# Kernel tuning notes

Hardware: AMD Instinct MI355X
Metric: run time of the kernel (lower is better)

Reference implementation:

```python
import jax, jax.numpy as jnp
import numpy as np


def setup_inputs() -> dict:
    key = jax.random.key(0)
    kq, kv = jax.random.split(key)
    B, Lq, Lv, H = 8, 2048, 2048, 256
    query = jax.random.normal(kq, (B, Lq, H), dtype=jnp.float32)
    value = jax.random.normal(kv, (B, Lv, H), dtype=jnp.float32)
    return {"query": query, "value": value}


def reference(query, value):
    # score[b, q, v] = sum_h query[b, q, h] * value[b, v, h]
    score = jnp.einsum("bqh,bvh->bqv", query, value)
    # softmax over the value axis (last dim), numerically stable
    attn = jax.nn.softmax(score, axis=-1)
    # context[b, q, h] = sum_v attn[b, q, v] * value[b, v, h]
    context = jnp.einsum("bqv,bvh->bqh", attn, value)
    return (context, attn)
```

## Files before the change

kernel.cpp:

```cpp
#include <hip/hip_runtime.h>
#include <hip/hip_bf16.h>

#define LQ 2048
#define LV 2048
#define NH 256
#define NB 8

typedef __attribute__((ext_vector_type(4))) float f32x4;
typedef __attribute__((ext_vector_type(8))) short bf16x8;

__device__ __forceinline__ ushort f32_bf16(float x) {
  union { float f; unsigned u; } c; c.f = x;
  unsigned r = (c.u + 0x7FFFu + ((c.u >> 16) & 1u)) >> 16;
  return (ushort)r;
}
__device__ __forceinline__ float bf16_f32(ushort h) {
  union { unsigned u; float f; } c; c.u = ((unsigned)h) << 16;
  return c.f;
}
__device__ __forceinline__ void gl_lds16(const ushort* g, ushort* l) {
  __builtin_amdgcn_global_load_lds(
      (const __attribute__((address_space(1))) unsigned int*)(g),
      (__attribute__((address_space(3))) unsigned int*)(l), 16, 0, 0);
}


__global__ __launch_bounds__(256) void k_prepQ(
    const float* __restrict__ Q, ushort* __restrict__ Qh, ushort* __restrict__ Ql) {
  int i = blockIdx.x * 256 + threadIdx.x;
  float4 x = reinterpret_cast<const float4*>(Q)[i];
  ushort4 h, l;
  h.x = f32_bf16(x.x); l.x = f32_bf16(x.x - bf16_f32(h.x));
  h.y = f32_bf16(x.y); l.y = f32_bf16(x.y - bf16_f32(h.y));
  h.z = f32_bf16(x.z); l.z = f32_bf16(x.z - bf16_f32(h.z));
  h.w = f32_bf16(x.w); l.w = f32_bf16(x.w - bf16_f32(h.w));
  reinterpret_cast<ushort4*>(Qh)[i] = h;
  reinterpret_cast<ushort4*>(Ql)[i] = l;
}

__global__ __launch_bounds__(256) void k_prepV(
    const float* __restrict__ V, ushort* __restrict__ Vh, ushort* __restrict__ Vl,
    ushort* __restrict__ VhT) {
  int id = blockIdx.x;
  int b = id & 7, vt = (id >> 3) & 31, ht = id >> 8;
  __shared__ ushort sT[64][72];
  int t = threadIdx.x;
  const size_t base = ((size_t)(b * LV) + vt * 64) * NH + ht * 64;
  int r0 = t >> 4, c4 = (t & 15) << 2;
  #pragma unroll
  for (int it = 0; it < 4; ++it) {
    int r = r0 + it * 16;
    size_t off = base + (size_t)r * NH + c4;
    float4 x = *reinterpret_cast<const float4*>(V + off);
    ushort4 h, l;
    h.x = f32_bf16(x.x); l.x = f32_bf16(x.x - bf16_f32(h.x));
    h.y = f32_bf16(x.y); l.y = f32_bf16(x.y - bf16_f32(h.y));
    h.z = f32_bf16(x.z); l.z = f32_bf16(x.z - bf16_f32(h.z));
    h.w = f32_bf16(x.w); l.w = f32_bf16(x.w - bf16_f32(h.w));
    *reinterpret_cast<ushort4*>(Vh + off) = h;
    *reinterpret_cast<ushort4*>(Vl + off) = l;
    *reinterpret_cast<ushort4*>(&sT[r][c4]) = h;
  }
  __syncthreads();
  int hh = t & 63, vc = t >> 6;
  ushort tmp[16];
  #pragma unroll
  for (int j = 0; j < 16; ++j) tmp[j] = sT[vc * 16 + j][hh];
  ushort* dst = VhT + ((size_t)(b * NH) + ht * 64 + hh) * LV + vt * 64 + vc * 16;
  *reinterpret_cast<ushort4*>(dst)      = *reinterpret_cast<ushort4*>(&tmp[0]);
  *reinterpret_cast<ushort4*>(dst + 4)  = *reinterpret_cast<ushort4*>(&tmp[4]);
  *reinterpret_cast<ushort4*>(dst + 8)  = *reinterpret_cast<ushort4*>(&tmp[8]);
  *reinterpret_cast<ushort4*>(dst + 12) = *reinterpret_cast<ushort4*>(&tmp[12]);
}

__global__ __launch_bounds__(512) void k_scores6(
    const ushort* __restrict__ Qh, const ushort* __restrict__ Ql,
    const ushort* __restrict__ Vh, const ushort* __restrict__ Vl,
    float* __restrict__ S, float2* __restrict__ PS) {
  extern __shared__ ushort dynlds[];
  int id = blockIdx.x;
  int b = id & 7, qt = (id >> 3) & 7, vt = id >> 6;
  int t = threadIdx.x, lane = t & 63, w = t >> 6;

  const size_t bq = (size_t)(b * LQ) + qt * 256;
  const size_t bv = (size_t)(b * LV) + vt * 256;

#define LBASE(buf, arr) ((char*)dynlds + ((buf) * 4 + (arr)) * (256 * 64))

#define STAGE(buf, kt)                                                      \
  {                                                                         \
    int krow = t >> 2, c = t & 3;                                           \
    _Pragma("unroll")                                                       \
    for (int hh = 0; hh < 2; ++hh) {                                        \
      int row = hh * 128 + krow;                                            \
      int csrc = c ^ ((row >> 1) & 3);                                      \
      size_t gq = (bq + row) * NH + (kt) * 32 + csrc * 8;                   \
      size_t gv = (bv + row) * NH + (kt) * 32 + csrc * 8;                   \
      gl_lds16(Qh + gq, (ushort*)(LBASE(buf, 0) + row * 64 + c * 16));      \
      gl_lds16(Ql + gq, (ushort*)(LBASE(buf, 1) + row * 64 + c * 16));      \
      gl_lds16(Vh + gv, (ushort*)(LBASE(buf, 2) + row * 64 + c * 16));      \
      gl_lds16(Vl + gv, (ushort*)(LBASE(buf, 3) + row * 64 + c * 16));      \
    }                                                                       \
  }

  int wq = w >> 1, wv = w & 1;
  int ar = wq * 64 + (lane & 15);
  int br = wv * 128 + (lane & 15);
  int kb = lane >> 4;

  f32x4 acc[4][8] = {};

  STAGE(0, 0);
  STAGE(1, 1);

  #pragma unroll
  for (int kt = 0; kt < 8; ++kt) {
    const int cur = kt & 1;
    if (kt < 7) { asm volatile("s_waitcnt vmcnt(8)" ::: "memory"); }
    else        { asm volatile("s_waitcnt vmcnt(0)" ::: "memory"); }
    __builtin_amdgcn_sched_barrier(0);
    __builtin_amdgcn_s_barrier();
    __builtin_amdgcn_sched_barrier(0);

    bf16x8 ah[4], al[4];
    #pragma unroll
    for (int m = 0; m < 4; ++m) {
      int r = ar + m * 16;
      int off = r * 64 + ((kb ^ ((r >> 1) & 3)) << 4);
      ah[m] = *reinterpret_cast<const bf16x8*>(LBASE(cur, 0) + off);
      al[m] = *reinterpret_cast<const bf16x8*>(LBASE(cur, 1) + off);
    }
    __builtin_amdgcn_s_setprio(1);
    #pragma unroll
    for (int n = 0; n < 8; ++n) {
      int r = br + n * 16;
      int off = r * 64 + ((kb ^ ((r >> 1) & 3)) << 4);
      bf16x8 bh = *reinterpret_cast<const bf16x8*>(LBASE(cur, 2) + off);
      bf16x8 bl = *reinterpret_cast<const bf16x8*>(LBASE(cur, 3) + off);
      #pragma unroll
      for (int m = 0; m < 4; ++m) {
        acc[m][n] = __builtin_amdgcn_mfma_f32_16x16x32_bf16(ah[m], bh, acc[m][n], 0, 0, 0);
        acc[m][n] = __builtin_amdgcn_mfma_f32_16x16x32_bf16(ah[m], bl, acc[m][n], 0, 0, 0);
        acc[m][n] = __builtin_amdgcn_mfma_f32_16x16x32_bf16(al[m], bh, acc[m][n], 0, 0, 0);
      }
    }
    __builtin_amdgcn_s_setprio(0);
    __builtin_amdgcn_sched_barrier(0);
    __builtin_amdgcn_s_barrier();
    __builtin_amdgcn_sched_barrier(0);
    if (kt < 6) STAGE(cur, kt + 2);
  }

  #pragma unroll
  for (int m = 0; m < 4; ++m) {
    #pragma unroll
    for (int j = 0; j < 4; ++j) {
      float mx = acc[m][0][j];
      #pragma unroll
      for (int n = 1; n < 8; ++n) mx = fmaxf(mx, acc[m][n][j]);
      #pragma unroll
      for (int off = 1; off < 16; off <<= 1) mx = fmaxf(mx, __shfl_xor(mx, off));
      float s = 0.f;
      #pragma unroll
      for (int n = 0; n < 8; ++n) s += __expf(acc[m][n][j] - mx);
      #pragma unroll
      for (int off = 1; off < 16; off <<= 1) s += __shfl_xor(s, off);
      if ((lane & 15) == 0) {
        int g = lane >> 4;
        int row = wq * 64 + m * 16 + g * 4 + j;
        float2 v; v.x = mx; v.y = s;
        PS[((size_t)(b * LQ) + qt * 256 + row) * 16 + vt * 2 + wv] = v;
      }
    }
  }

  float* Sp = S + (size_t)b * LQ * LV + (size_t)(qt * 256 + wq * 64) * LV
            + vt * 256 + wv * 128;
  int rb = (lane >> 4) << 2, c0 = lane & 15;
  #pragma unroll
  for (int m = 0; m < 4; ++m)
    #pragma unroll
    for (int j = 0; j < 4; ++j)
      #pragma unroll
      for (int n = 0; n < 8; ++n)
        Sp[(size_t)(m * 16 + rb + j) * LV + n * 16 + c0] = acc[m][n][j];
#undef STAGE
#undef LBASE
}

__global__ __launch_bounds__(512) void k_ctx8(
    const ushort* __restrict__ VhT, const float2* __restrict__ PS,
    float* __restrict__ A, float* __restrict__ C) {
  int id = blockIdx.x;
  int b = id & 7, qs = id >> 3;
  __shared__ float lm[32], li[32];
  __shared__ __align__(16) ushort sP[4][32 * 64];

  int t = threadIdx.x, lane = t & 63, w = t >> 6;
  float* Ab = A + (size_t)b * LQ * LV + (size_t)qs * 32 * LV;
  const ushort* Vb = VhT + (size_t)b * NH * LV;

  const int prow = t >> 4, pc = (t & 15) << 2;
  float* aaddr = Ab + (size_t)prow * LV + pc;
  const int poff = (prow * 128 + pc * 2) ^ ((prow & 7) << 4);

  {
    int row = t >> 4, seg = t & 15;
    float2 p = PS[((size_t)(b * LQ) + qs * 32 + row) * 16 + seg];
    float M = p.x, s = p.y;
    #pragma unroll
    for (int off = 1; off < 16; off <<= 1) {
      float mo = __shfl_xor(M, off), so = __shfl_xor(s, off);
      float mn = fmaxf(M, mo);
      s = s * __expf(M - mn) + so * __expf(mo - mn);
      M = mn;
    }
    if (seg == 0) { lm[row] = M; li[row] = 1.f / s; }
  }
  __syncthreads();

  const float pm = lm[prow], pinv = li[prow];

#define PRODUCE(xv, v0, buf)                                                \
  {                                                                         \
    float4 p;                                                               \
    p.x = __expf((xv).x - pm) * pinv; p.y = __expf((xv).y - pm) * pinv;     \
    p.z = __expf((xv).z - pm) * pinv; p.w = __expf((xv).w - pm) * pinv;     \
    *reinterpret_cast<float4*>(aaddr + (v0)) = p;                           \
    ushort4 pk;                                                             \
    pk.x = f32_bf16(p.x); pk.y = f32_bf16(p.y);                             \
    pk.z = f32_bf16(p.z); pk.w = f32_bf16(p.w);                             \
    *reinterpret_cast<ushort4*>((char*)&sP[buf][0] + poff) = pk;            \
  }

  float4 x0 = *reinterpret_cast<const float4*>(aaddr);
  float4 x1 = *reinterpret_cast<const float4*>(aaddr + 64);
  PRODUCE(x0, 0, 0);
  PRODUCE(x1, 64, 1);
  x0 = *reinterpret_cast<const float4*>(aaddr + 128);
  x1 = *reinterpret_cast<const float4*>(aaddr + 192);
  __syncthreads();

  f32x4 acc[2][2] = {};
  const int NP = LV / 128;

  for (int p = 0; p < NP; ++p) {
    const int cur = (p & 1) << 1;
    const int nxt = cur ^ 2;
    const int v0 = p * 128;
    if (p + 1 < NP) {
      PRODUCE(x0, v0 + 128, nxt);
      PRODUCE(x1, v0 + 192, nxt + 1);
    }
    if (p + 2 < NP) {
      x0 = *reinterpret_cast<const float4*>(aaddr + v0 + 256);
      x1 = *reinterpret_cast<const float4*>(aaddr + v0 + 320);
    }

    #pragma unroll
    for (int c = 0; c < 2; ++c) {
      #pragma unroll
      for (int ks = 0; ks < 2; ++ks) {
        int vbyte = ks * 64 + ((lane >> 4) << 4);
        bf16x8 pa[2];
        #pragma unroll
        for (int i2 = 0; i2 < 2; ++i2) {
          int arow = i2 * 16 + (lane & 15);
          pa[i2] = *reinterpret_cast<const bf16x8*>(
              (char*)&sP[cur + c][0] + ((arow * 128 + vbyte) ^ ((arow & 7) << 4)));
        }
        #pragma unroll
        for (int n = 0; n < 2; ++n) {
          int hrow = w * 32 + n * 16 + (lane & 15);
          bf16x8 vb = *reinterpret_cast<const bf16x8*>(
              Vb + (size_t)hrow * LV + v0 + c * 64 + ks * 32 + ((lane >> 4) << 3));
          #pragma unroll
          for (int i2 = 0; i2 < 2; ++i2)
            acc[i2][n] = __builtin_amdgcn_mfma_f32_16x16x32_bf16(pa[i2], vb, acc[i2][n], 0, 0, 0);
        }
      }
    }
    __syncthreads();
  }
#undef PRODUCE

  float* Cb = C + ((size_t)b * LQ + qs * 32) * NH + w * 32;
  int rb = (lane >> 4) << 2, c0 = lane & 15;
  #pragma unroll
  for (int i2 = 0; i2 < 2; ++i2)
    #pragma unroll
    for (int j = 0; j < 4; ++j)
      #pragma unroll
      for (int n = 0; n < 2; ++n)
        Cb[(size_t)(i2 * 16 + rb + j) * NH + n * 16 + c0] = acc[i2][n][j];
}


__global__ __launch_bounds__(256) void k_scores_fb(
    const float* __restrict__ Q, const float* __restrict__ V,
    float* __restrict__ S) {
  int id = blockIdx.x;
  int b = id & 7;
  int inner = id >> 3;
  int qt = inner & 31;
  int vt = inner >> 5;
  __shared__ ushort sQh[64 * 64], sQl[64 * 64], sVh[64 * 64], sVl[64 * 64];
  const float* Qb = Q + (size_t)(b * LQ + qt * 64) * NH;
  const float* Vb = V + (size_t)(b * LV + vt * 64) * NH;
  const int t = threadIdx.x;
  const int lane = t & 63;
  const int w = t >> 6;
  f32x4 acc[4] = {};
  const int row0 = t >> 4;
  const int col4 = (t & 15) << 2;
  for (int kc = 0; kc < 4; ++kc) {
    #pragma unroll
    for (int it = 0; it < 4; ++it) {
      int row = row0 + (it << 4);
      const float4 qx = *reinterpret_cast<const float4*>(Qb + (size_t)row * NH + kc * 64 + col4);
      const float4 vx = *reinterpret_cast<const float4*>(Vb + (size_t)row * NH + kc * 64 + col4);
      int off = ((row * 128 + col4 * 2) ^ ((row & 7) << 4)) >> 1;
      ushort4 h, l;
      h.x = f32_bf16(qx.x); l.x = f32_bf16(qx.x - bf16_f32(h.x));
      h.y = f32_bf16(qx.y); l.y = f32_bf16(qx.y - bf16_f32(h.y));
      h.z = f32_bf16(qx.z); l.z = f32_bf16(qx.z - bf16_f32(h.z));
      h.w = f32_bf16(qx.w); l.w = f32_bf16(qx.w - bf16_f32(h.w));
      *reinterpret_cast<ushort4*>(&sQh[off]) = h;
      *reinterpret_cast<ushort4*>(&sQl[off]) = l;
      h.x = f32_bf16(vx.x); l.x = f32_bf16(vx.x - bf16_f32(h.x));
      h.y = f32_bf16(vx.y); l.y = f32_bf16(vx.y - bf16_f32(h.y));
      h.z = f32_bf16(vx.z); l.z = f32_bf16(vx.z - bf16_f32(h.z));
      h.w = f32_bf16(vx.w); l.w = f32_bf16(vx.w - bf16_f32(h.w));
      *reinterpret_cast<ushort4*>(&sVh[off]) = h;
      *reinterpret_cast<ushort4*>(&sVl[off]) = l;
    }
    __syncthreads();
    int arow = (w << 4) + (lane & 15);
    int abase = arow * 128;
    int aswz = (arow & 7) << 4;
    #pragma unroll
    for (int ks = 0; ks < 2; ++ks) {
      int koffB = (ks << 6) + ((lane >> 4) << 4);
      int aoff = ((abase + koffB) ^ aswz) >> 1;
      bf16x8 ah = *reinterpret_cast<const bf16x8*>(&sQh[aoff]);
      bf16x8 al = *reinterpret_cast<const bf16x8*>(&sQl[aoff]);
      #pragma unroll
      for (int n = 0; n < 4; ++n) {
        int brow = (n << 4) + (lane & 15);
        int boff = (((brow * 128) + koffB) ^ ((brow & 7) << 4)) >> 1;
        bf16x8 bh = *reinterpret_cast<const bf16x8*>(&sVh[boff]);
        bf16x8 bl = *reinterpret_cast<const bf16x8*>(&sVl[boff]);
        acc[n] = __builtin_amdgcn_mfma_f32_16x16x32_bf16(ah, bh, acc[n], 0, 0, 0);
        acc[n] = __builtin_amdgcn_mfma_f32_16x16x32_bf16(ah, bl, acc[n], 0, 0, 0);
        acc[n] = __builtin_amdgcn_mfma_f32_16x16x32_bf16(al, bh, acc[n], 0, 0, 0);
      }
    }
    __syncthreads();
  }
  float* Sp = S + (size_t)b * LQ * LV + (size_t)(qt * 64) * LV + vt * 64;
  int rbase = (w << 4) + ((lane >> 4) << 2);
  int c0 = lane & 15;
  #pragma unroll
  for (int n = 0; n < 4; ++n)
    #pragma unroll
    for (int j = 0; j < 4; ++j)
      Sp[(size_t)(rbase + j) * LV + (n << 4) + c0] = acc[n][j];
}

__global__ __launch_bounds__(256) void k_stats_fb(const float* __restrict__ S,
                                                  float* __restrict__ ml) {
  const size_t r = blockIdx.x;
  const float* row = S + r * LV;
  int t = threadIdx.x;
  float4 a = *reinterpret_cast<const float4*>(row + (t << 2));
  float4 c = *reinterpret_cast<const float4*>(row + 1024 + (t << 2));
  float m = fmaxf(fmaxf(fmaxf(a.x, a.y), fmaxf(a.z, a.w)),
                  fmaxf(fmaxf(c.x, c.y), fmaxf(c.z, c.w)));
  #pragma unroll
  for (int off = 32; off; off >>= 1) m = fmaxf(m, __shfl_xor(m, off));
  __shared__ float redm[4];
  __shared__ float reds[4];
  if ((t & 63) == 0) redm[t >> 6] = m;
  __syncthreads();
  m = fmaxf(fmaxf(redm[0], redm[1]), fmaxf(redm[2], redm[3]));
  float s = __expf(a.x - m) + __expf(a.y - m) + __expf(a.z - m) + __expf(a.w - m)
          + __expf(c.x - m) + __expf(c.y - m) + __expf(c.z - m) + __expf(c.w - m);
  #pragma unroll
  for (int off = 32; off; off >>= 1) s += __shfl_xor(s, off);
  if ((t & 63) == 0) reds[t >> 6] = s;
  __syncthreads();
  if (t == 0) {
    float tot = reds[0] + reds[1] + reds[2] + reds[3];
    ml[2 * r] = m;
    ml[2 * r + 1] = 1.0f / tot;
  }
}

__global__ __launch_bounds__(256) void k_ctx_fb(
    const float* __restrict__ V, const float* __restrict__ ml,
    float* __restrict__ A, float* __restrict__ C) {
  int id = blockIdx.x;
  int b = id & 7;
  int qt = id >> 3;
  __shared__ ushort sP[32 * 40];
  __shared__ ushort sVT[256 * 40];
  __shared__ float lmv[32], liv[32];
  int t = threadIdx.x;
  int lane = t & 63;
  int w = t >> 6;
  int wr = w >> 1, wh = w & 1;
  if (t < 32) {
    size_t r = (size_t)b * LQ + qt * 32 + t;
    lmv[t] = ml[2 * r];
    liv[t] = ml[2 * r + 1];
  }
  __syncthreads();
  f32x4 acc[8] = {};
  float* Ab = A + (size_t)b * LQ * LV + (size_t)(qt * 32) * LV;
  const float* Vb = V + (size_t)b * LV * NH;
  const int prow = t >> 3;
  const int pv4 = (t & 7) << 2;
  for (int v0 = 0; v0 < LV; v0 += 32) {
    {
      float* addr = Ab + (size_t)prow * LV + v0 + pv4;
      float4 s4 = *reinterpret_cast<const float4*>(addr);
      float m = lmv[prow], inv = liv[prow];
      float4 p4;
      p4.x = __expf(s4.x - m) * inv;
      p4.y = __expf(s4.y - m) * inv;
      p4.z = __expf(s4.z - m) * inv;
      p4.w = __expf(s4.w - m) * inv;
      *reinterpret_cast<float4*>(addr) = p4;
      ushort4 pb;
      pb.x = f32_bf16(p4.x); pb.y = f32_bf16(p4.y);
      pb.z = f32_bf16(p4.z); pb.w = f32_bf16(p4.w);
      *reinterpret_cast<ushort4*>(&sP[prow * 40 + pv4]) = pb;
    }
    #pragma unroll 4
    for (int vl = 0; vl < 32; ++vl) {
      float x = Vb[(size_t)(v0 + vl) * NH + t];
      sVT[t * 40 + vl] = f32_bf16(x);
    }
    __syncthreads();
    bf16x8 pa = *reinterpret_cast<const bf16x8*>(
        &sP[((wr << 4) + (lane & 15)) * 40 + ((lane >> 4) << 3)]);
    #pragma unroll
    for (int n = 0; n < 8; ++n) {
      int hrow = (wh << 7) + (n << 4) + (lane & 15);
      bf16x8 vb = *reinterpret_cast<const bf16x8*>(
          &sVT[hrow * 40 + ((lane >> 4) << 3)]);
      acc[n] = __builtin_amdgcn_mfma_f32_16x16x32_bf16(pa, vb, acc[n], 0, 0, 0);
    }
    __syncthreads();
  }
  float* Cb = C + ((size_t)b * LQ + qt * 32) * NH;
  int rbase = (wr << 4) + ((lane >> 4) << 2);
  int c0 = lane & 15;
  #pragma unroll
  for (int n = 0; n < 8; ++n)
    #pragma unroll
    for (int j = 0; j < 4; ++j)
      Cb[(size_t)(rbase + j) * NH + (wh << 7) + (n << 4) + c0] = acc[n][j];
}


extern "C" void kernel_launch(void* const* d_in, const int* in_sizes, int n_in,
                              void* d_out, int out_size, void* d_ws, size_t ws_size,
                              hipStream_t stream) {
  const float* Q = (const float*)d_in[0];
  const float* V = (const float*)d_in[1];
  float* out = (float*)d_out;
  float* C = out;
  float* A = out + (size_t)NB * LQ * NH;

  const size_t NE = (size_t)NB * LQ * NH;
  const size_t PSN = (size_t)NB * LQ * 16;
  const size_t need = NE * 2 * 5 + PSN * 8;
  const int DYN_LDS = 2 * 4 * 256 * 32 * 2;

  bool big_lds_ok =
      hipFuncSetAttribute((const void*)k_scores6,
                          hipFuncAttributeMaxDynamicSharedMemorySize,
                          DYN_LDS) == hipSuccess;

  if (ws_size >= need && big_lds_ok) {
    ushort* Qh  = (ushort*)d_ws;
    ushort* Ql  = Qh + NE;
    ushort* Vh  = Ql + NE;
    ushort* Vl  = Vh + NE;
    ushort* VhT = Vl + NE;
    float2* PS  = (float2*)(VhT + NE);
    k_prepQ<<<dim3(NE / 4 / 256), dim3(256), 0, stream>>>(Q, Qh, Ql);
    k_prepV<<<dim3(NB * 32 * 4), dim3(256), 0, stream>>>(V, Vh, Vl, VhT);
    k_scores6<<<dim3(NB * 8 * 8), dim3(512), DYN_LDS, stream>>>(Qh, Ql, Vh, Vl, A, PS);
    k_ctx8<<<dim3(NB * 64), dim3(512), 0, stream>>>(VhT, PS, A, C);
  } else {
    float* ml = (float*)d_ws;
    k_scores_fb<<<dim3(NB * 32 * 32), dim3(256), 0, stream>>>(Q, V, A);
    k_stats_fb<<<dim3(NB * LQ), dim3(256), 0, stream>>>(A, ml);
    k_ctx_fb<<<dim3(NB * 64), dim3(256), 0, stream>>>(V, ml, A, C);
  }
}
```

Baseline: 161.1 us.

## Store unnormalized fp16 exp scores in-place to halve intermediate score traffic

The scores kernel now computes exp(score - local segment max) and writes it as fp16 into the upper half of each attention row, instead of writing raw fp32 scores. The context kernel reads these fp16 values and rescales them by a per-segment factor built from the partial max/sum stats. It then writes final fp32 probabilities in place. This cuts the bytes written and re-read for the large intermediate score matrix and drops the exp from the context kernel. In exchange it adds fp16 rounding and underflow on the probabilities, and it depends on in-place reads staying ahead of writes within each row.

```diff
diff --git a/kernel.cpp b/kernel.cpp
--- a/kernel.cpp
+++ b/kernel.cpp
@@ -17,6 +17,12 @@
 __device__ __forceinline__ float bf16_f32(ushort h) {
   union { unsigned u; float f; } c; c.u = ((unsigned)h) << 16;
   return c.f;
+}
+__device__ __forceinline__ ushort f32_f16(float x) {
+  union { _Float16 h; ushort u; } c; c.h = (_Float16)x; return c.u;
+}
+__device__ __forceinline__ float f16_f32(ushort u) {
+  union { ushort u; _Float16 h; } c; c.u = u; return (float)c.h;
 }
 __device__ __forceinline__ void gl_lds16(const ushort* g, ushort* l) {
   __builtin_amdgcn_global_load_lds(
@@ -73,7 +79,7 @@
   *reinterpret_cast<ushort4*>(dst + 12) = *reinterpret_cast<ushort4*>(&tmp[12]);
 }
 
-__global__ __launch_bounds__(512) void k_scores6(
+__global__ __launch_bounds__(512) void k_scores7(
     const ushort* __restrict__ Qh, const ushort* __restrict__ Ql,
     const ushort* __restrict__ Vh, const ushort* __restrict__ Vl,
     float* __restrict__ S, float2* __restrict__ PS) {
@@ -151,6 +157,7 @@
     if (kt < 6) STAGE(cur, kt + 2);
   }
 
+  const int g = lane >> 4, c0 = lane & 15;
   #pragma unroll
   for (int m = 0; m < 4; ++m) {
     #pragma unroll
@@ -160,40 +167,33 @@
       for (int n = 1; n < 8; ++n) mx = fmaxf(mx, acc[m][n][j]);
       #pragma unroll
       for (int off = 1; off < 16; off <<= 1) mx = fmaxf(mx, __shfl_xor(mx, off));
+      float e[8];
       float s = 0.f;
       #pragma unroll
-      for (int n = 0; n < 8; ++n) s += __expf(acc[m][n][j] - mx);
+      for (int n = 0; n < 8; ++n) { e[n] = __expf(acc[m][n][j] - mx); s += e[n]; }
       #pragma unroll
       for (int off = 1; off < 16; off <<= 1) s += __shfl_xor(s, off);
-      if ((lane & 15) == 0) {
-        int g = lane >> 4;
-        int row = wq * 64 + m * 16 + g * 4 + j;
+      int row = qt * 256 + wq * 64 + m * 16 + g * 4 + j;
+      if (c0 == 0) {
         float2 v; v.x = mx; v.y = s;
-        PS[((size_t)(b * LQ) + qt * 256 + row) * 16 + vt * 2 + wv] = v;
+        PS[((size_t)(b * LQ) + row) * 16 + vt * 2 + wv] = v;
       }
-    }
-  }
-
-  float* Sp = S + (size_t)b * LQ * LV + (size_t)(qt * 256 + wq * 64) * LV
-            + vt * 256 + wv * 128;
-  int rb = (lane >> 4) << 2, c0 = lane & 15;
-  #pragma unroll
-  for (int m = 0; m < 4; ++m)
-    #pragma unroll
-    for (int j = 0; j < 4; ++j)
-      #pragma unroll
-      for (int n = 0; n < 8; ++n)
-        Sp[(size_t)(m * 16 + rb + j) * LV + n * 16 + c0] = acc[m][n][j];
+      ushort* pr = (ushort*)(S + ((size_t)(b * LQ) + row) * LV + 1024);
+      int cb = vt * 256 + wv * 128 + c0;
+      #pragma unroll
+      for (int n = 0; n < 8; ++n) pr[cb + n * 16] = f32_f16(e[n]);
+    }
+  }
 #undef STAGE
 #undef LBASE
 }
 
-__global__ __launch_bounds__(512) void k_ctx8(
+__global__ __launch_bounds__(512) void k_ctx10(
     const ushort* __restrict__ VhT, const float2* __restrict__ PS,
     float* __restrict__ A, float* __restrict__ C) {
   int id = blockIdx.x;
   int b = id & 7, qs = id >> 3;
-  __shared__ float lm[32], li[32];
+  __shared__ float lf[32][16];
   __shared__ __align__(16) ushort sP[4][32 * 64];
 
   int t = threadIdx.x, lane = t & 63, w = t >> 6;
@@ -202,6 +202,7 @@
 
   const int prow = t >> 4, pc = (t & 15) << 2;
   float* aaddr = Ab + (size_t)prow * LV + pc;
+  const ushort* a16 = (const ushort*)(Ab + (size_t)prow * LV + 1024) + pc;
   const int poff = (prow * 128 + pc * 2) ^ ((prow & 7) << 4);
 
   {
@@ -215,17 +216,15 @@
       s = s * __expf(M - mn) + so * __expf(mo - mn);
       M = mn;
     }
-    if (seg == 0) { lm[row] = M; li[row] = 1.f / s; }
+    lf[row][seg] = __expf(p.x - M) / s;
   }
   __syncthreads();
 
-  const float pm = lm[prow], pinv = li[prow];
-
-#define PRODUCE(xv, v0, buf)                                                \
+#define PRODUCE(xv, v0, buf, fac)                                           \
   {                                                                         \
     float4 p;                                                               \
-    p.x = __expf((xv).x - pm) * pinv; p.y = __expf((xv).y - pm) * pinv;     \
-    p.z = __expf((xv).z - pm) * pinv; p.w = __expf((xv).w - pm) * pinv;     \
+    p.x = f16_f32((xv).x) * (fac); p.y = f16_f32((xv).y) * (fac);           \
+    p.z = f16_f32((xv).z) * (fac); p.w = f16_f32((xv).w) * (fac);           \
     *reinterpret_cast<float4*>(aaddr + (v0)) = p;                           \
     ushort4 pk;                                                             \
     pk.x = f32_bf16(p.x); pk.y = f32_bf16(p.y);                             \
@@ -233,12 +232,15 @@
     *reinterpret_cast<ushort4*>((char*)&sP[buf][0] + poff) = pk;            \
   }
 
-  float4 x0 = *reinterpret_cast<const float4*>(aaddr);
-  float4 x1 = *reinterpret_cast<const float4*>(aaddr + 64);
-  PRODUCE(x0, 0, 0);
-  PRODUCE(x1, 64, 1);
-  x0 = *reinterpret_cast<const float4*>(aaddr + 128);
-  x1 = *reinterpret_cast<const float4*>(aaddr + 192);
+  ushort4 x0 = *reinterpret_cast<const ushort4*>(a16);
+  ushort4 x1 = *reinterpret_cast<const ushort4*>(a16 + 64);
+  {
+    float f0 = lf[prow][0];
+    PRODUCE(x0, 0, 0, f0);
+    PRODUCE(x1, 64, 1, f0);
+  }
+  x0 = *reinterpret_cast<const ushort4*>(a16 + 128);
+  x1 = *reinterpret_cast<const ushort4*>(a16 + 192);
   __syncthreads();
 
   f32x4 acc[2][2] = {};
@@ -249,12 +251,13 @@
     const int nxt = cur ^ 2;
     const int v0 = p * 128;
     if (p + 1 < NP) {
-      PRODUCE(x0, v0 + 128, nxt);
-      PRODUCE(x1, v0 + 192, nxt + 1);
+      float fn = lf[prow][p + 1];
+      PRODUCE(x0, v0 + 128, nxt, fn);
+      PRODUCE(x1, v0 + 192, nxt + 1, fn);
     }
     if (p + 2 < NP) {
-      x0 = *reinterpret_cast<const float4*>(aaddr + v0 + 256);
-      x1 = *reinterpret_cast<const float4*>(aaddr + v0 + 320);
+      x0 = *reinterpret_cast<const ushort4*>(a16 + v0 + 256);
+      x1 = *reinterpret_cast<const ushort4*>(a16 + v0 + 320);
     }
 
     #pragma unroll
@@ -479,7 +482,7 @@
   const int DYN_LDS = 2 * 4 * 256 * 32 * 2;
 
   bool big_lds_ok =
-      hipFuncSetAttribute((const void*)k_scores6,
+      hipFuncSetAttribute((const void*)k_scores7,
                           hipFuncAttributeMaxDynamicSharedMemorySize,
                           DYN_LDS) == hipSuccess;
 
@@ -492,8 +495,8 @@
     float2* PS  = (float2*)(VhT + NE);
     k_prepQ<<<dim3(NE / 4 / 256), dim3(256), 0, stream>>>(Q, Qh, Ql);
     k_prepV<<<dim3(NB * 32 * 4), dim3(256), 0, stream>>>(V, Vh, Vl, VhT);
-    k_scores6<<<dim3(NB * 8 * 8), dim3(512), DYN_LDS, stream>>>(Qh, Ql, Vh, Vl, A, PS);
-    k_ctx8<<<dim3(NB * 64), dim3(512), 0, stream>>>(VhT, PS, A, C);
+    k_scores7<<<dim3(NB * 8 * 8), dim3(512), DYN_LDS, stream>>>(Qh, Ql, Vh, Vl, A, PS);
+    k_ctx10<<<dim3(NB * 64), dim3(512), 0, stream>>>(VhT, PS, A, C);
   } else {
     float* ml = (float*)d_ws;
     k_scores_fb<<<dim3(NB * 32 * 32), dim3(256), 0, stream>>>(Q, V, A);
```

Result: faster. 146.8 us (-8.9%).
